# Optimization experiments

Measured on AMD Instinct MI355X. Metric: run time of the kernel, lower is better.

## Reference

```python
import jax, jax.numpy as jnp
import numpy as np

N_NODES = 25000
IN_DIM = 16
EDGE_DIM = 8
HID = 32
OUT_DIM = 16
N_EDGES = 400000
MLP_HID = 32


def setup_inputs() -> dict:
    key = jax.random.key(0)
    ks = jax.random.split(key, 12)
    x = jax.random.normal(ks[0], (N_NODES, IN_DIM), dtype=jnp.float32)
    edge_index = jax.random.randint(ks[1], (2, N_EDGES), 0, N_NODES, dtype=jnp.int32)
    edge_attr = jax.random.normal(ks[2], (N_EDGES, EDGE_DIM), dtype=jnp.float32)
    s = lambda fan_in: 1.0 / np.sqrt(fan_in)
    W1 = jax.random.uniform(ks[3], (EDGE_DIM, MLP_HID), minval=-s(EDGE_DIM), maxval=s(EDGE_DIM))
    b1 = jax.random.uniform(ks[4], (MLP_HID,), minval=-s(EDGE_DIM), maxval=s(EDGE_DIM))
    W2 = jax.random.uniform(ks[5], (MLP_HID, IN_DIM * HID), minval=-s(MLP_HID), maxval=s(MLP_HID))
    b2 = jax.random.uniform(ks[6], (IN_DIM * HID,), minval=-s(MLP_HID), maxval=s(MLP_HID))
    root = jax.random.uniform(ks[7], (IN_DIM, HID), minval=-s(IN_DIM), maxval=s(IN_DIM))
    bias = jnp.zeros((HID,), dtype=jnp.float32)
    Wlin = jax.random.uniform(ks[8], (HID, OUT_DIM), minval=-s(HID), maxval=s(HID))
    blin = jax.random.uniform(ks[9], (OUT_DIM,), minval=-s(HID), maxval=s(HID))
    return {"x": x, "edge_attr": edge_attr, "W1": W1, "b1": b1, "W2": W2,
            "b2": b2, "root": root, "bias": bias, "Wlin": Wlin, "blin": blin,
            "edge_index": edge_index}


def reference(x, edge_attr, W1, b1, W2, b2, root, bias, Wlin, blin, edge_index):
    src, dst = edge_index[0], edge_index[1]  # x_j gathered from src, aggregated at dst
    # edge MLP -> per-edge weight matrix [E, IN_DIM, HID]
    h = jax.nn.relu(edge_attr @ W1 + b1)
    W_e = (h @ W2 + b2).reshape(-1, IN_DIM, HID)
    # gather source features and per-edge matvec: [E, HID]
    msg = jnp.einsum('ei,eio->eo', x[src], W_e)
    # scatter-mean over target nodes
    agg = jax.ops.segment_sum(msg, dst, num_segments=N_NODES)
    cnt = jax.ops.segment_sum(jnp.ones((msg.shape[0],), dtype=msg.dtype), dst, num_segments=N_NODES)
    agg = agg / jnp.maximum(cnt, 1.0)[:, None]
    # NNConv root weight + bias, then ReLU and final linear
    out = jax.nn.relu(agg + x @ root + bias)
    return out @ Wlin + blin
```

## Files before the change

kernel.cpp:

```cpp
#include <hip/hip_runtime.h>
#include <cstdint>

#define E_EDGES 400000
#define N_NODES 25000
#define NU      12500
#define NPACK   18432
#define HBLOCKS 391
#define EBLK    1563
#define NWAVES  (EBLK*4)

typedef float  f32x4  __attribute__((ext_vector_type(4)));
typedef __bf16 bf16x8 __attribute__((ext_vector_type(8)));

static __device__ __forceinline__ ushort f2bf(float f) {
    union { __bf16 b; ushort u; } c; c.b = (__bf16)f; return c.u;
}

__global__ void __launch_bounds__(256) k_pre(const float* __restrict__ W2,
                                             const float* __restrict__ b2,
                                             const float* __restrict__ W1,
                                             ushort* __restrict__ packed,
                                             uint* __restrict__ zbase) {
    const int t = blockIdx.x * 256 + threadIdx.x;
    for (int i = t; i < 1000000; i += EBLK * 256) zbase[i] = 0u;
    if (t >= NPACK) return;
    float v = 0.0f;
    if (t < 17408) {
        int j  = t & 7;
        int ln = (t >> 3) & 15;
        int kg = (t >> 7) & 3;
        int nt = (t >> 9) & 1;
        int kt = t >> 10;
        int kap = (j < 4) ? (kg * 4 + j) : (16 + kg * 4 + (j - 4));
        if (kt < 16)       v = W2[kap * 512 + kt * 32 + nt * 16 + ln];
        else if (kap < 16) v = b2[kap * 32 + nt * 16 + ln];
    } else {
        int idx  = t - 17408;
        int half = idx >> 9;
        int lane = (idx >> 3) & 63;
        int j    = idx & 7;
        int kg = lane >> 4, ln = lane & 15;
        if (kg == 0) v = W1[j * 32 + half * 16 + ln];
    }
    packed[t] = f2bf(v);
}

__global__ void __launch_bounds__(256) k_edge(const float* __restrict__ ea,
                                              const float* __restrict__ x,
                                              const int* __restrict__ ei,
                                              const ushort* __restrict__ packed,
                                              const float* __restrict__ b1,
                                              float* __restrict__ agg,
                                              uint* __restrict__ cnt8) {
    if (blockIdx.x < HBLOCKS) {
        const int base = blockIdx.x * 1024 + threadIdx.x * 4;
        if (base < E_EDGES) {
            const int4 dv = *(const int4*)(ei + E_EDGES + base);
            atomicAdd(&cnt8[dv.x * 8 + ((base + 0) & 7)], 1u);
            atomicAdd(&cnt8[dv.y * 8 + ((base + 1) & 7)], 1u);
            atomicAdd(&cnt8[dv.z * 8 + ((base + 2) & 7)], 1u);
            atomicAdd(&cnt8[dv.w * 8 + ((base + 3) & 7)], 1u);
        }
        return;
    }

    __shared__ alignas(16) ushort w2l[NPACK];
    __shared__ float b1l[32];
    {
        const uint4* s = (const uint4*)packed;
        uint4* d = (uint4*)w2l;
        for (int i = threadIdx.x; i < NPACK / 8; i += 256) d[i] = s[i];
        if (threadIdx.x < 32) b1l[threadIdx.x] = b1[threadIdx.x];
    }
    __syncthreads();

    const int lane = threadIdx.x & 63;
    const int ln = lane & 15;
    const int kg = lane >> 4;
    const int wid = (blockIdx.x - HBLOCKS) * 4 + (threadIdx.x >> 6);

    const bf16x8 aw0 = *(const bf16x8*)(&w2l[17408 + lane * 8]);
    const bf16x8 aw1 = *(const bf16x8*)(&w2l[17408 + 512 + lane * 8]);
    const f32x4 z4 = {0.f, 0.f, 0.f, 0.f};
    const __bf16 zb = (__bf16)0.0f;

    int u = wid;
    int s0 = ei[u * 32 + ln];
    int s1 = ei[u * 32 + 16 + ln];
    int4 d0 = *(const int4*)(ei + E_EDGES + u * 32 + kg * 4);
    int4 d1 = *(const int4*)(ei + E_EDGES + u * 32 + 16 + kg * 4);
    const f32x4* ep0 = (const f32x4*)(ea + (size_t)(u * 32 + ln) * 8);
    f32x4 ea00 = ep0[0], ea01 = ep0[1];
    const f32x4* ep1 = (const f32x4*)(ea + (size_t)(u * 32 + 16 + ln) * 8);
    f32x4 ea10 = ep1[0], ea11 = ep1[1];

#pragma unroll
    for (int it = 0; it < 2; ++it) {
        const int un = u + NWAVES;
        const bool pf = (it == 0) && (un < NU);

        const f32x4* xp0 = (const f32x4*)(x + (size_t)s0 * 16);
        const f32x4 xa0 = xp0[0], xa1 = xp0[1], xa2 = xp0[2], xa3 = xp0[3];
        const f32x4* xp1 = (const f32x4*)(x + (size_t)s1 * 16);
        const f32x4 xb0 = xp1[0], xb1 = xp1[1], xb2 = xp1[2], xb3 = xp1[3];

        int ns0 = 0, ns1 = 0;
        int4 nd0 = {0,0,0,0}, nd1 = {0,0,0,0};
        f32x4 nea00 = z4, nea01 = z4, nea10 = z4, nea11 = z4;
        if (pf) {
            ns0 = ei[un * 32 + ln];
            ns1 = ei[un * 32 + 16 + ln];
            nd0 = *(const int4*)(ei + E_EDGES + un * 32 + kg * 4);
            nd1 = *(const int4*)(ei + E_EDGES + un * 32 + 16 + kg * 4);
            const f32x4* np0 = (const f32x4*)(ea + (size_t)(un * 32 + ln) * 8);
            nea00 = np0[0]; nea01 = np0[1];
            const f32x4* np1 = (const f32x4*)(ea + (size_t)(un * 32 + 16 + ln) * 8);
            nea10 = np1[0]; nea11 = np1[1];
        }

        bf16x8 eb0, eb1;
        if (kg == 0) {
            eb0[0]=(__bf16)ea00[0]; eb0[1]=(__bf16)ea00[1]; eb0[2]=(__bf16)ea00[2]; eb0[3]=(__bf16)ea00[3];
            eb0[4]=(__bf16)ea01[0]; eb0[5]=(__bf16)ea01[1]; eb0[6]=(__bf16)ea01[2]; eb0[7]=(__bf16)ea01[3];
            eb1[0]=(__bf16)ea10[0]; eb1[1]=(__bf16)ea10[1]; eb1[2]=(__bf16)ea10[2]; eb1[3]=(__bf16)ea10[3];
            eb1[4]=(__bf16)ea11[0]; eb1[5]=(__bf16)ea11[1]; eb1[6]=(__bf16)ea11[2]; eb1[7]=(__bf16)ea11[3];
        } else {
            eb0[0]=zb; eb0[1]=zb; eb0[2]=zb; eb0[3]=zb; eb0[4]=zb; eb0[5]=zb; eb0[6]=zb; eb0[7]=zb;
            eb1 = eb0;
        }
        f32x4 hA0 = __builtin_amdgcn_mfma_f32_16x16x32_bf16(aw0, eb0, z4, 0, 0, 0);
        f32x4 hA1 = __builtin_amdgcn_mfma_f32_16x16x32_bf16(aw1, eb0, z4, 0, 0, 0);
        f32x4 hB0 = __builtin_amdgcn_mfma_f32_16x16x32_bf16(aw0, eb1, z4, 0, 0, 0);
        f32x4 hB1 = __builtin_amdgcn_mfma_f32_16x16x32_bf16(aw1, eb1, z4, 0, 0, 0);

        float h0[8], h1[8];
#pragma unroll
        for (int r = 0; r < 4; ++r) {
            const float blo = b1l[4 * kg + r], bhi = b1l[16 + 4 * kg + r];
            h0[r]     = fmaxf(hA0[r] + blo, 0.f);
            h0[4 + r] = fmaxf(hA1[r] + bhi, 0.f);
            h1[r]     = fmaxf(hB0[r] + blo, 0.f);
            h1[4 + r] = fmaxf(hB1[r] + bhi, 0.f);
        }

        float xr0[16], xr1[16];
        xr0[0]=xa0[0]; xr0[1]=xa0[1]; xr0[2]=xa0[2]; xr0[3]=xa0[3];
        xr0[4]=xa1[0]; xr0[5]=xa1[1]; xr0[6]=xa1[2]; xr0[7]=xa1[3];
        xr0[8]=xa2[0]; xr0[9]=xa2[1]; xr0[10]=xa2[2]; xr0[11]=xa2[3];
        xr0[12]=xa3[0]; xr0[13]=xa3[1]; xr0[14]=xa3[2]; xr0[15]=xa3[3];
        xr1[0]=xb0[0]; xr1[1]=xb0[1]; xr1[2]=xb0[2]; xr1[3]=xb0[3];
        xr1[4]=xb1[0]; xr1[5]=xb1[1]; xr1[6]=xb1[2]; xr1[7]=xb1[3];
        xr1[8]=xb2[0]; xr1[9]=xb2[1]; xr1[10]=xb2[2]; xr1[11]=xb2[3];
        xr1[12]=xb3[0]; xr1[13]=xb3[1]; xr1[14]=xb3[2]; xr1[15]=xb3[3];

        f32x4 acc00 = z4, acc01 = z4, acc10 = z4, acc11 = z4;

#pragma unroll
        for (int kt = 0; kt < 16; ++kt) {
            const bf16x8 bf0 = *(const bf16x8*)(&w2l[(kt * 2 + 0) * 512 + lane * 8]);
            const bf16x8 bf1 = *(const bf16x8*)(&w2l[(kt * 2 + 1) * 512 + lane * 8]);
            const float xv0 = xr0[kt], xv1 = xr1[kt];
            bf16x8 a0, a1;
#pragma unroll
            for (int j = 0; j < 8; ++j) {
                a0[j] = (__bf16)(xv0 * h0[j]);
                a1[j] = (__bf16)(xv1 * h1[j]);
            }
            acc00 = __builtin_amdgcn_mfma_f32_16x16x32_bf16(a0, bf0, acc00, 0, 0, 0);
            acc10 = __builtin_amdgcn_mfma_f32_16x16x32_bf16(a1, bf0, acc10, 0, 0, 0);
            acc01 = __builtin_amdgcn_mfma_f32_16x16x32_bf16(a0, bf1, acc01, 0, 0, 0);
            acc11 = __builtin_amdgcn_mfma_f32_16x16x32_bf16(a1, bf1, acc11, 0, 0, 0);
        }
        {
            const f32x4 xs0 = (kg == 0) ? xa0 : ((kg == 1) ? xa1 : ((kg == 2) ? xa2 : xa3));
            const f32x4 xs1 = (kg == 0) ? xb0 : ((kg == 1) ? xb1 : ((kg == 2) ? xb2 : xb3));
            bf16x8 a0, a1;
            a0[0]=(__bf16)xs0[0]; a0[1]=(__bf16)xs0[1]; a0[2]=(__bf16)xs0[2]; a0[3]=(__bf16)xs0[3];
            a0[4]=zb; a0[5]=zb; a0[6]=zb; a0[7]=zb;
            a1[0]=(__bf16)xs1[0]; a1[1]=(__bf16)xs1[1]; a1[2]=(__bf16)xs1[2]; a1[3]=(__bf16)xs1[3];
            a1[4]=zb; a1[5]=zb; a1[6]=zb; a1[7]=zb;
            const bf16x8 bf0 = *(const bf16x8*)(&w2l[(16 * 2 + 0) * 512 + lane * 8]);
            const bf16x8 bf1 = *(const bf16x8*)(&w2l[(16 * 2 + 1) * 512 + lane * 8]);
            acc00 = __builtin_amdgcn_mfma_f32_16x16x32_bf16(a0, bf0, acc00, 0, 0, 0);
            acc10 = __builtin_amdgcn_mfma_f32_16x16x32_bf16(a1, bf0, acc10, 0, 0, 0);
            acc01 = __builtin_amdgcn_mfma_f32_16x16x32_bf16(a0, bf1, acc01, 0, 0, 0);
            acc11 = __builtin_amdgcn_mfma_f32_16x16x32_bf16(a1, bf1, acc11, 0, 0, 0);
        }

        atomicAdd(&agg[d0.x * 32 + ln],      acc00[0]);
        atomicAdd(&agg[d0.y * 32 + ln],      acc00[1]);
        atomicAdd(&agg[d0.z * 32 + ln],      acc00[2]);
        atomicAdd(&agg[d0.w * 32 + ln],      acc00[3]);
        atomicAdd(&agg[d0.x * 32 + 16 + ln], acc01[0]);
        atomicAdd(&agg[d0.y * 32 + 16 + ln], acc01[1]);
        atomicAdd(&agg[d0.z * 32 + 16 + ln], acc01[2]);
        atomicAdd(&agg[d0.w * 32 + 16 + ln], acc01[3]);
        atomicAdd(&agg[d1.x * 32 + ln],      acc10[0]);
        atomicAdd(&agg[d1.y * 32 + ln],      acc10[1]);
        atomicAdd(&agg[d1.z * 32 + ln],      acc10[2]);
        atomicAdd(&agg[d1.w * 32 + ln],      acc10[3]);
        atomicAdd(&agg[d1.x * 32 + 16 + ln], acc11[0]);
        atomicAdd(&agg[d1.y * 32 + 16 + ln], acc11[1]);
        atomicAdd(&agg[d1.z * 32 + 16 + ln], acc11[2]);
        atomicAdd(&agg[d1.w * 32 + 16 + ln], acc11[3]);

        if (!pf) break;
        u = un;
        s0 = ns0; s1 = ns1; d0 = nd0; d1 = nd1;
        ea00 = nea00; ea01 = nea01; ea10 = nea10; ea11 = nea11;
    }
}

__global__ void __launch_bounds__(256) k_node(const float* __restrict__ agg,
                                              const uint* __restrict__ cnt8,
                                              const float* __restrict__ x,
                                              const float* __restrict__ root,
                                              const float* __restrict__ bias,
                                              const float* __restrict__ Wlin,
                                              const float* __restrict__ blin,
                                              float* __restrict__ out) {
    __shared__ float al[256];
    const int n0 = blockIdx.x * 8;
    const int t = threadIdx.x;
    const int n = n0 + (t >> 5), h = t & 31;
    float a = 0.0f;
    if (n < N_NODES) {
        const uint4 c0 = *(const uint4*)(cnt8 + (size_t)n * 8);
        const uint4 c1 = *(const uint4*)(cnt8 + (size_t)n * 8 + 4);
        const float c = (float)(c0.x + c0.y + c0.z + c0.w + c1.x + c1.y + c1.z + c1.w);
        float s = agg[n * 32 + h] / fmaxf(c, 1.0f) + bias[h];
        const f32x4* xp = (const f32x4*)(x + (size_t)n * 16);
        const f32x4 x0 = xp[0], x1 = xp[1], x2 = xp[2], x3 = xp[3];
        float xv[16];
        xv[0]=x0[0]; xv[1]=x0[1]; xv[2]=x0[2]; xv[3]=x0[3];
        xv[4]=x1[0]; xv[5]=x1[1]; xv[6]=x1[2]; xv[7]=x1[3];
        xv[8]=x2[0]; xv[9]=x2[1]; xv[10]=x2[2]; xv[11]=x2[3];
        xv[12]=x3[0]; xv[13]=x3[1]; xv[14]=x3[2]; xv[15]=x3[3];
#pragma unroll
        for (int i = 0; i < 16; ++i) s += xv[i] * root[i * 32 + h];
        a = fmaxf(s, 0.0f);
    }
    al[t] = a;
    __syncthreads();
    if (t < 128) {
        const int nj = n0 + (t >> 4), j = t & 15;
        if (nj < N_NODES) {
            float s = blin[j];
#pragma unroll
            for (int h2 = 0; h2 < 32; ++h2) s += al[(t >> 4) * 32 + h2] * Wlin[h2 * 16 + j];
            out[nj * 16 + j] = s;
        }
    }
}

extern "C" void kernel_launch(void* const* d_in, const int* in_sizes, int n_in,
                              void* d_out, int out_size, void* d_ws, size_t ws_size,
                              hipStream_t stream) {
    const float* x    = (const float*)d_in[0];
    const float* ea   = (const float*)d_in[1];
    const float* W1   = (const float*)d_in[2];
    const float* b1   = (const float*)d_in[3];
    const float* W2   = (const float*)d_in[4];
    const float* b2   = (const float*)d_in[5];
    const float* root = (const float*)d_in[6];
    const float* bias = (const float*)d_in[7];
    const float* Wlin = (const float*)d_in[8];
    const float* blin = (const float*)d_in[9];
    const int*   ei   = (const int*)d_in[10];
    float* out = (float*)d_out;

    char* ws = (char*)d_ws;
    float*  agg    = (float*)(ws + 0);
    uint*   cnt8   = (uint*)(ws + 3200000);
    ushort* packed = (ushort*)(ws + 4000000);

    k_pre<<<EBLK, 256, 0, stream>>>(W2, b2, W1, packed, (uint*)ws);
    k_edge<<<HBLOCKS + EBLK, 256, 0, stream>>>(ea, x, ei, packed, b1, agg, cnt8);
    k_node<<<3125, 256, 0, stream>>>(agg, cnt8, x, root, bias, Wlin, blin, out);
}
```

Measured before the change: 75.65 us.

## Accumulate scatter sums with packed bf16x2 atomics instead of fp32 atomics

The aggregation buffer is stored as bf16, and each lane pair exchanges values through shuffles so one packed v2bf16 atomic add covers two adjacent columns. This halves the number of global atomics and the size of the zeroed and read-back aggregation buffer. In exchange, sums accumulated in bf16 lose precision, and with many edges per node this can exceed the output tolerance.

```diff
diff --git a/kernel.cpp b/kernel.cpp
--- a/kernel.cpp
+++ b/kernel.cpp
@@ -11,9 +11,23 @@
 
 typedef float  f32x4  __attribute__((ext_vector_type(4)));
 typedef __bf16 bf16x8 __attribute__((ext_vector_type(8)));
+typedef short  s16x2  __attribute__((ext_vector_type(2)));
 
 static __device__ __forceinline__ ushort f2bf(float f) {
     union { __bf16 b; ushort u; } c; c.b = (__bf16)f; return c.u;
+}
+static __device__ __forceinline__ float bf2f(uint32_t u) {
+    union { uint32_t u; float f; } v; v.u = u << 16; return v.f;
+}
+static __device__ __forceinline__ uint pk2(float a, float b) {
+    return (uint)f2bf(a) | ((uint)f2bf(b) << 16);
+}
+static __device__ __forceinline__ void atom_pk_bf16(ushort* p, uint v) {
+    s16x2 sv;
+    sv[0] = (short)(v & 0xffffu);
+    sv[1] = (short)(v >> 16);
+    __builtin_amdgcn_global_atomic_fadd_v2bf16(
+        (__attribute__((address_space(1))) s16x2*)p, sv);
 }
 
 __global__ void __launch_bounds__(256) k_pre(const float* __restrict__ W2,
@@ -22,7 +36,7 @@
                                              ushort* __restrict__ packed,
                                              uint* __restrict__ zbase) {
     const int t = blockIdx.x * 256 + threadIdx.x;
-    for (int i = t; i < 1000000; i += EBLK * 256) zbase[i] = 0u;
+    for (int i = t; i < 600000; i += EBLK * 256) zbase[i] = 0u;
     if (t >= NPACK) return;
     float v = 0.0f;
     if (t < 17408) {
@@ -50,7 +64,7 @@
                                               const int* __restrict__ ei,
                                               const ushort* __restrict__ packed,
                                               const float* __restrict__ b1,
-                                              float* __restrict__ agg,
+                                              ushort* __restrict__ aggbf,
                                               uint* __restrict__ cnt8) {
     if (blockIdx.x < HBLOCKS) {
         const int base = blockIdx.x * 1024 + threadIdx.x * 4;
@@ -83,6 +97,9 @@
     const bf16x8 aw1 = *(const bf16x8*)(&w2l[17408 + 512 + lane * 8]);
     const f32x4 z4 = {0.f, 0.f, 0.f, 0.f};
     const __bf16 zb = (__bf16)0.0f;
+
+    const bool ev = (ln & 1) == 0;
+    const int colb = ln & ~1;
 
     int u = wid;
     int s0 = ei[u * 32 + ln];
@@ -187,22 +204,20 @@
             acc11 = __builtin_amdgcn_mfma_f32_16x16x32_bf16(a1, bf1, acc11, 0, 0, 0);
         }
 
-        atomicAdd(&agg[d0.x * 32 + ln],      acc00[0]);
-        atomicAdd(&agg[d0.y * 32 + ln],      acc00[1]);
-        atomicAdd(&agg[d0.z * 32 + ln],      acc00[2]);
-        atomicAdd(&agg[d0.w * 32 + ln],      acc00[3]);
-        atomicAdd(&agg[d0.x * 32 + 16 + ln], acc01[0]);
-        atomicAdd(&agg[d0.y * 32 + 16 + ln], acc01[1]);
-        atomicAdd(&agg[d0.z * 32 + 16 + ln], acc01[2]);
-        atomicAdd(&agg[d0.w * 32 + 16 + ln], acc01[3]);
-        atomicAdd(&agg[d1.x * 32 + ln],      acc10[0]);
-        atomicAdd(&agg[d1.y * 32 + ln],      acc10[1]);
-        atomicAdd(&agg[d1.z * 32 + ln],      acc10[2]);
-        atomicAdd(&agg[d1.w * 32 + ln],      acc10[3]);
-        atomicAdd(&agg[d1.x * 32 + 16 + ln], acc11[0]);
-        atomicAdd(&agg[d1.y * 32 + 16 + ln], acc11[1]);
-        atomicAdd(&agg[d1.z * 32 + 16 + ln], acc11[2]);
-        atomicAdd(&agg[d1.w * 32 + 16 + ln], acc11[3]);
+#pragma unroll
+        for (int r = 0; r < 4; ++r) {
+            const float a0v = acc00[r], b0v = acc10[r];
+            const float a1v = acc01[r], b1v = acc11[r];
+            const float pa0 = __shfl_xor(a0v, 1), pb0 = __shfl_xor(b0v, 1);
+            const float pa1 = __shfl_xor(a1v, 1), pb1 = __shfl_xor(b1v, 1);
+            const int drow = ev
+                ? ((r == 0) ? d0.x : (r == 1) ? d0.y : (r == 2) ? d0.z : d0.w)
+                : ((r == 0) ? d1.x : (r == 1) ? d1.y : (r == 2) ? d1.z : d1.w);
+            const uint v0 = ev ? pk2(a0v, pa0) : pk2(pb0, b0v);
+            const uint v1 = ev ? pk2(a1v, pa1) : pk2(pb1, b1v);
+            atom_pk_bf16(aggbf + (size_t)drow * 32 + colb,      v0);
+            atom_pk_bf16(aggbf + (size_t)drow * 32 + 16 + colb, v1);
+        }
 
         if (!pf) break;
         u = un;
@@ -211,7 +226,7 @@
     }
 }
 
-__global__ void __launch_bounds__(256) k_node(const float* __restrict__ agg,
+__global__ void __launch_bounds__(256) k_node(const ushort* __restrict__ aggbf,
                                               const uint* __restrict__ cnt8,
                                               const float* __restrict__ x,
                                               const float* __restrict__ root,
@@ -228,7 +243,7 @@
         const uint4 c0 = *(const uint4*)(cnt8 + (size_t)n * 8);
         const uint4 c1 = *(const uint4*)(cnt8 + (size_t)n * 8 + 4);
         const float c = (float)(c0.x + c0.y + c0.z + c0.w + c1.x + c1.y + c1.z + c1.w);
-        float s = agg[n * 32 + h] / fmaxf(c, 1.0f) + bias[h];
+        float s = bf2f(aggbf[(size_t)n * 32 + h]) / fmaxf(c, 1.0f) + bias[h];
         const f32x4* xp = (const f32x4*)(x + (size_t)n * 16);
         const f32x4 x0 = xp[0], x1 = xp[1], x2 = xp[2], x3 = xp[3];
         float xv[16];
@@ -270,11 +285,11 @@
     float* out = (float*)d_out;
 
     char* ws = (char*)d_ws;
-    float*  agg    = (float*)(ws + 0);
-    uint*   cnt8   = (uint*)(ws + 3200000);
-    ushort* packed = (ushort*)(ws + 4000000);
+    ushort* aggbf  = (ushort*)(ws + 0);
+    uint*   cnt8   = (uint*)(ws + 1600000);
+    ushort* packed = (ushort*)(ws + 2400000);
 
     k_pre<<<EBLK, 256, 0, stream>>>(W2, b2, W1, packed, (uint*)ws);
-    k_edge<<<HBLOCKS + EBLK, 256, 0, stream>>>(ea, x, ei, packed, b1, agg, cnt8);
-    k_node<<<3125, 256, 0, stream>>>(agg, cnt8, x, root, bias, Wlin, blin, out);
-}
+    k_edge<<<HBLOCKS + EBLK, 256, 0, stream>>>(ea, x, ei, packed, b1, aggbf, cnt8);
+    k_node<<<3125, 256, 0, stream>>>(aggbf, cnt8, x, root, bias, Wlin, blin, out);
+}
```

New measurement: 75.76 us. No clear change (+0.1%).
